# Kernel tuning notes

Hardware: AMD Instinct MI355X
Metric: run time of the kernel (lower is better)

Reference implementation:

```python
import jax, jax.numpy as jnp
import numpy as np

EMBED_DIM = 1024
NUM_HEADS = 16
HEAD_DIM = EMBED_DIM // NUM_HEADS
B, S = 4, 1024
EPS = 1e-5
NEG = -1e9


def layer_norm(h, gamma, beta):
    mu = jnp.mean(h, axis=-1, keepdims=True)
    var = jnp.mean(jnp.square(h - mu), axis=-1, keepdims=True)
    return (h - mu) * jax.lax.rsqrt(var + EPS) * gamma + beta


def setup_inputs() -> dict:
    key = jax.random.key(0)
    ks = jax.random.split(key, 8)
    scale = 1.0 / np.sqrt(EMBED_DIM)
    x = jax.random.normal(ks[0], (B, S, EMBED_DIM), dtype=jnp.float32)
    mask = jax.random.randint(ks[1], (B, S, S), 0, 2).astype(jnp.bool_)
    Wq = jax.random.uniform(ks[2], (EMBED_DIM, EMBED_DIM), jnp.float32, -scale, scale)
    bq = jax.random.uniform(ks[3], (EMBED_DIM,), jnp.float32, -scale, scale)
    Wk = jax.random.uniform(ks[4], (EMBED_DIM, EMBED_DIM), jnp.float32, -scale, scale)
    bk = jax.random.uniform(ks[5], (EMBED_DIM,), jnp.float32, -scale, scale)
    gq = jnp.ones((EMBED_DIM,), jnp.float32)
    bq_n = jnp.zeros((EMBED_DIM,), jnp.float32)
    gk = jnp.ones((EMBED_DIM,), jnp.float32)
    bk_n = jnp.zeros((EMBED_DIM,), jnp.float32)
    return {"x": x, "mask": mask, "Wq": Wq, "bq": bq, "Wk": Wk, "bk": bk,
            "gq": gq, "bq_n": bq_n, "gk": gk, "bk_n": bk_n}


def reference(x, mask, Wq, bq, Wk, bk, gq, bq_n, gk, bk_n):
    b, s, _ = x.shape
    # proj -> LayerNorm -> ReLU, split heads: [B,S,H,D]
    Q = jax.nn.relu(layer_norm(x @ Wq + bq, gq, bq_n)).reshape(b, s, NUM_HEADS, HEAD_DIM)
    K = jax.nn.relu(layer_norm(x @ Wk + bk, gk, bk_n)).reshape(b, s, NUM_HEADS, HEAD_DIM)
    # scores [B,H,S,S]
    scores = jnp.einsum('bqhd,bkhd->bhqk', Q, K) / np.sqrt(HEAD_DIM).astype(np.float32)
    # symmetric masking: mask applied along keys, then (via transpose trick) along queries
    m = (mask | jnp.swapaxes(mask, -1, -2))[:, None, :, :]
    scores = jnp.where(m, NEG, scores)
    attn = jax.nn.softmax(scores, axis=-1)
    return attn.mean(axis=1)  # [B,S,S]
```

## Files before the change

kernel.cpp:

```cpp
#include <hip/hip_runtime.h>
#include <hip/hip_bf16.h>

#define B_ 4
#define S_ 1024
#define E_ 1024
#define H_ 16
#define D_ 64

typedef __attribute__((ext_vector_type(8))) short short8;
typedef __attribute__((ext_vector_type(4))) float f32x4;

static __device__ __forceinline__ unsigned short f2bf(float x) {
  unsigned int u = __float_as_uint(x);
  unsigned int r = u + 0x7fffu + ((u >> 16) & 1u);
  return (unsigned short)(r >> 16);
}
static __device__ __forceinline__ float bf2f(unsigned short b) {
  return __uint_as_float((unsigned int)b << 16);
}

#define GL2LDS16(g, l)                                                            \
  __builtin_amdgcn_global_load_lds(                                               \
      (const __attribute__((address_space(1))) unsigned int*)(g),                 \
      (__attribute__((address_space(3))) unsigned int*)(l), 16, 0, 0)

__global__ __launch_bounds__(256) void prep_kernel(const int* __restrict__ mask,
                                                   const float* __restrict__ x,
                                                   const float* __restrict__ Wq,
                                                   const float* __restrict__ Wk,
                                                   unsigned char* __restrict__ msym,
                                                   unsigned short* __restrict__ xbf,
                                                   unsigned short* __restrict__ Wt) {
  __shared__ __align__(16) char u_lds[32 * 33 * 4];
  const int blk = blockIdx.x;
  const int tid = threadIdx.x;
  if (blk < 4096) {
    int (*T)[33] = (int(*)[33])u_lds;
    const int b = blk >> 10;
    const int rest = blk & 1023;
    const int i0 = (rest >> 5) << 5;
    const int j0 = (rest & 31) << 5;
    const int ii = tid >> 3;
    const int jj4 = (tid & 7) << 2;
    const size_t bO = (size_t)b * S_ * S_;
    const int4 m2 = *(const int4*)&mask[bO + (size_t)(j0 + ii) * S_ + i0 + jj4];
    T[ii][jj4 + 0] = m2.x; T[ii][jj4 + 1] = m2.y; T[ii][jj4 + 2] = m2.z; T[ii][jj4 + 3] = m2.w;
    __syncthreads();
    const int4 m1 = *(const int4*)&mask[bO + (size_t)(i0 + ii) * S_ + j0 + jj4];
    uchar4 o;
    o.x = ((m1.x != 0) || (T[jj4 + 0][ii] != 0)) ? 1 : 0;
    o.y = ((m1.y != 0) || (T[jj4 + 1][ii] != 0)) ? 1 : 0;
    o.z = ((m1.z != 0) || (T[jj4 + 2][ii] != 0)) ? 1 : 0;
    o.w = ((m1.w != 0) || (T[jj4 + 3][ii] != 0)) ? 1 : 0;
    *(uchar4*)&msym[bO + (size_t)(i0 + ii) * S_ + j0 + jj4] = o;
  } else if (blk < 6144) {
    const size_t i = ((size_t)(blk - 4096) * 256 + tid) * 8;
    const float4 a = *(const float4*)(x + i);
    const float4 b = *(const float4*)(x + i + 4);
    const ushort4 p0 = {f2bf(a.x), f2bf(a.y), f2bf(a.z), f2bf(a.w)};
    const ushort4 p1 = {f2bf(b.x), f2bf(b.y), f2bf(b.z), f2bf(b.w)};
    *(ushort4*)(xbf + i) = p0;
    *(ushort4*)(xbf + i + 4) = p1;
  } else {
    unsigned short (*T2)[36] = (unsigned short(*)[36])u_lds;
    const int wblk = blk - 6144;
    const int mat = wblk >> 10;
    const int kt = (wblk >> 5) & 31, ntb = wblk & 31;
    const float* W = mat ? Wk : Wq;
    const int r = tid >> 3, c4 = (tid & 7) << 2;
    const float4 v = *(const float4*)&W[(size_t)(kt * 32 + r) * 1024 + ntb * 32 + c4];
    T2[r][c4 + 0] = f2bf(v.x); T2[r][c4 + 1] = f2bf(v.y);
    T2[r][c4 + 2] = f2bf(v.z); T2[r][c4 + 3] = f2bf(v.w);
    __syncthreads();
    const ushort4 o = {T2[c4 + 0][r], T2[c4 + 1][r], T2[c4 + 2][r], T2[c4 + 3][r]};
    *(ushort4*)&Wt[(size_t)(mat * 1024 + ntb * 32 + r) * 1024 + kt * 32 + c4] = o;
  }
}

__global__ __launch_bounds__(256) void gemm_mfma_kernel(const unsigned short* __restrict__ Abf,
                                                        const unsigned short* __restrict__ Wt,
                                                        unsigned short* __restrict__ P,
                                                        int nstride) {
  __shared__ __align__(16) unsigned short As[128 * 32];
  __shared__ __align__(16) unsigned short Bs[128 * 32];
  const int tid = threadIdx.x;
  const int m0 = (blockIdx.x & 31) << 7;
  const int n0 = (blockIdx.x >> 5) << 7;
  const int wave = tid >> 6, lane = tid & 63;
  const int ln15 = lane & 15, rg = lane >> 4;
  const int wm = (wave & 1) << 6;
  const int wn = (wave >> 1) << 6;
  const int sr = tid >> 2;
  const int sc = (tid & 3) << 3;
  const unsigned short* gA = Abf + (size_t)(m0 + sr) * 1024 + sc;
  const unsigned short* gB = Wt + (size_t)(n0 + sr) * 1024 + sc;
  unsigned short* lA = As + tid * 8;
  unsigned short* lB = Bs + tid * 8;
  f32x4 acc[4][4];
#pragma unroll
  for (int i = 0; i < 4; ++i)
#pragma unroll
    for (int j = 0; j < 4; ++j) acc[i][j] = (f32x4){0.0f, 0.0f, 0.0f, 0.0f};

  const unsigned short* pa = As + (wm + ln15) * 32 + rg * 8;
  const unsigned short* pb = Bs + (wn + ln15) * 32 + rg * 8;
  for (int k0 = 0; k0 < E_; k0 += 32) {
    GL2LDS16(gA + k0, lA);
    GL2LDS16(gA + k0 + (size_t)64 * 1024, lA + 2048);
    GL2LDS16(gB + k0, lB);
    GL2LDS16(gB + k0 + (size_t)64 * 1024, lB + 2048);
    __syncthreads();
    short8 af[4], bfr[4];
#pragma unroll
    for (int i = 0; i < 4; ++i) af[i] = *(const short8*)(pa + i * 16 * 32);
#pragma unroll
    for (int j = 0; j < 4; ++j) bfr[j] = *(const short8*)(pb + j * 16 * 32);
#pragma unroll
    for (int i = 0; i < 4; ++i)
#pragma unroll
      for (int j = 0; j < 4; ++j)
        acc[i][j] = __builtin_amdgcn_mfma_f32_16x16x32_bf16(af[i], bfr[j], acc[i][j], 0, 0, 0);
    __syncthreads();
  }
#pragma unroll
  for (int i = 0; i < 4; ++i)
#pragma unroll
    for (int j = 0; j < 4; ++j)
#pragma unroll
      for (int r = 0; r < 4; ++r) {
        const int row = m0 + wm + i * 16 + rg * 4 + r;
        const int col = n0 + wn + j * 16 + ln15;
        P[(size_t)row * nstride + col] = f2bf(acc[i][j][r]);
      }
}

__global__ __launch_bounds__(256) void ln_relu_bf_kernel(const unsigned short* __restrict__ P,
                                                         int rowstride, int coloff,
                                                         const float* __restrict__ bias,
                                                         const float* __restrict__ gamma,
                                                         const float* __restrict__ beta,
                                                         unsigned short* __restrict__ obf) {
  const int row = blockIdx.x;
  const int b = row >> 10, s = row & 1023;
  const unsigned short* p = P + (size_t)row * rowstride + coloff;
  const int tid = threadIdx.x;
  const ushort4 pv = *(const ushort4*)(p + tid * 4);
  float4 v = {bf2f(pv.x), bf2f(pv.y), bf2f(pv.z), bf2f(pv.w)};
  const float4 bb = ((const float4*)bias)[tid];
  v.x += bb.x; v.y += bb.y; v.z += bb.z; v.w += bb.w;
  float sum = v.x + v.y + v.z + v.w;
  float s2 = v.x * v.x + v.y * v.y + v.z * v.z + v.w * v.w;
#pragma unroll
  for (int off = 32; off >= 1; off >>= 1) {
    sum += __shfl_xor(sum, off);
    s2 += __shfl_xor(s2, off);
  }
  __shared__ float red[2][4];
  const int wave = tid >> 6, lane = tid & 63;
  if (lane == 0) { red[0][wave] = sum; red[1][wave] = s2; }
  __syncthreads();
  sum = red[0][0] + red[0][1] + red[0][2] + red[0][3];
  s2 = red[1][0] + red[1][1] + red[1][2] + red[1][3];
  const float mu = sum * (1.0f / E_);
  const float var = s2 * (1.0f / E_) - mu * mu;
  const float r = rsqrtf(var + 1e-5f);
  const float4 g = ((const float4*)gamma)[tid];
  const float4 bt = ((const float4*)beta)[tid];
  const float o0 = fmaxf((v.x - mu) * r * g.x + bt.x, 0.0f);
  const float o1 = fmaxf((v.y - mu) * r * g.y + bt.y, 0.0f);
  const float o2 = fmaxf((v.z - mu) * r * g.z + bt.z, 0.0f);
  const float o3 = fmaxf((v.w - mu) * r * g.w + bt.w, 0.0f);
  const int h = tid >> 4;
  const int d = (tid & 15) << 2;
  const ushort4 ob = {f2bf(o0), f2bf(o1), f2bf(o2), f2bf(o3)};
  *(ushort4*)&obf[((size_t)(b * H_ + h) * S_ + s) * D_ + d] = ob;
}

__global__ __launch_bounds__(1024, 4) void attn5_kernel(const unsigned short* __restrict__ Qbf,
                                                        const unsigned short* __restrict__ Kbf,
                                                        const unsigned char* __restrict__ msym,
                                                        float* __restrict__ out) {
  __shared__ __align__(16) unsigned short Qs[256 * 64];
  __shared__ __align__(16) unsigned short Ks[2][256 * 64];
  __shared__ __align__(16) float l_lds[16][16];
  __shared__ __align__(16) float linv[16];
  const int tid = threadIdx.x;
  const int wave = tid >> 6, lane = tid & 63;
  const int ln15 = lane & 15, rg = lane >> 4;
  const int b = blockIdx.x & 3;
  const int q0 = (blockIdx.x >> 2) << 4;

  const unsigned short* Kb = Kbf + (size_t)b * H_ * S_ * D_;

  {
    const int rho = tid >> 3, p = tid & 7;
    const int c = p ^ (rho & 7);
    const int rho2 = rho + 128;
    const int c2 = p ^ (rho2 & 7);
    const uint4 v0 = *(const uint4*)(Qbf + ((size_t)(b * H_ + (rho >> 4)) * S_ + q0 + (rho & 15)) * D_ + c * 8);
    const uint4 v1 = *(const uint4*)(Qbf + ((size_t)(b * H_ + (rho2 >> 4)) * S_ + q0 + (rho2 & 15)) * D_ + c2 * 8);
    *(uint4*)&Qs[rho * 64 + p * 8] = v0;
    *(uint4*)&Qs[rho2 * 64 + p * 8] = v1;
  }
  unsigned int mbits = 0;
#pragma unroll
  for (int qt = 0; qt < 4; ++qt)
#pragma unroll
    for (int r = 0; r < 4; ++r)
      mbits |= (msym[((size_t)b * S_ + q0 + rg * 4 + r) * S_ + qt * 256 + wave * 16 + ln15] ? 1u : 0u)
               << (qt * 4 + r);

  const int krow = tid >> 3, kp = tid & 7;
  const int kcc = kp ^ (krow & 7);
  {
    const unsigned short* src = Kb + (size_t)krow * D_ + kcc * 8;
    const uint4 p0 = *(const uint4*)src;
    const uint4 p1 = *(const uint4*)(src + 128 * D_);
    *(uint4*)&Ks[0][krow * 64 + kp * 8] = p0;
    *(uint4*)&Ks[0][(krow + 128) * 64 + kp * 8] = p1;
  }
  __syncthreads();

  const int pfrag = (rg ^ (ln15 & 7)) * 8;
  const unsigned short* QsW = Qs + ln15 * 64;
  const unsigned short* KsW0 = Ks[0] + (wave * 16 + ln15) * 64;
  const unsigned short* KsW1 = Ks[1] + (wave * 16 + ln15) * 64;

  float o[4][4] = {};
  unsigned int epack[4][2];
  uint4 pf0, pf1;

#pragma unroll 1
  for (int h = 0; h < 16; ++h) {
    const unsigned short* qrow = QsW + h * 16 * 64;
    const short8 a0 = *(const short8*)(qrow + pfrag);
    const short8 a1 = *(const short8*)(qrow + (pfrag ^ 32));
    float la[4] = {0.0f, 0.0f, 0.0f, 0.0f};
#pragma unroll
    for (int qt = 0; qt < 4; ++qt) {
      const int s = h * 4 + qt;
      if (s < 63) {
        const int s1 = s + 1;
        const unsigned short* src =
            Kb + ((size_t)(s1 >> 2) * S_ + ((s1 & 3) << 8) + krow) * D_ + kcc * 8;
        pf0 = *(const uint4*)src;
        pf1 = *(const uint4*)(src + 128 * D_);
      }
      const unsigned short* kw = (qt & 1) ? KsW1 : KsW0;
      const short8 b0 = *(const short8*)(kw + pfrag);
      const short8 b1 = *(const short8*)(kw + (pfrag ^ 32));
      f32x4 cc = {0.0f, 0.0f, 0.0f, 0.0f};
      cc = __builtin_amdgcn_mfma_f32_16x16x32_bf16(a0, b0, cc, 0, 0, 0);
      cc = __builtin_amdgcn_mfma_f32_16x16x32_bf16(a1, b1, cc, 0, 0, 0);
      float e[4];
#pragma unroll
      for (int r = 0; r < 4; ++r) {
        const float sv = fminf(cc[r] * 0.125f, 80.0f);
        e[r] = ((mbits >> (qt * 4 + r)) & 1u) ? 0.0f : __expf(sv);
        la[r] += e[r];
      }
      epack[qt][0] = (unsigned)f2bf(e[0]) | ((unsigned)f2bf(e[1]) << 16);
      epack[qt][1] = (unsigned)f2bf(e[2]) | ((unsigned)f2bf(e[3]) << 16);
      if (s < 63) {
        unsigned short* dst = (qt & 1) ? Ks[0] : Ks[1];
        *(uint4*)&dst[krow * 64 + kp * 8] = pf0;
        *(uint4*)&dst[(krow + 128) * 64 + kp * 8] = pf1;
      }
      if (qt < 3) __syncthreads();
    }
#pragma unroll
    for (int r = 0; r < 4; ++r) {
      float lv = la[r];
      lv += __shfl_xor(lv, 1);
      lv += __shfl_xor(lv, 2);
      lv += __shfl_xor(lv, 4);
      lv += __shfl_xor(lv, 8);
      la[r] = lv;
    }
    if (ln15 == 0) *(float4*)&l_lds[wave][rg * 4] = (float4){la[0], la[1], la[2], la[3]};
    __syncthreads();
    if (tid < 16) {
      float ssum = 0.0f;
#pragma unroll
      for (int w = 0; w < 16; ++w) ssum += l_lds[w][tid];
      linv[tid] = 0.0625f / ssum;
    }
    __syncthreads();
    const float4 li4 = *(const float4*)&linv[rg * 4];
#pragma unroll
    for (int qt = 0; qt < 4; ++qt) {
      o[qt][0] += __uint_as_float(epack[qt][0] << 16) * li4.x;
      o[qt][1] += __uint_as_float(epack[qt][0] & 0xFFFF0000u) * li4.y;
      o[qt][2] += __uint_as_float(epack[qt][1] << 16) * li4.z;
      o[qt][3] += __uint_as_float(epack[qt][1] & 0xFFFF0000u) * li4.w;
    }
  }
#pragma unroll
  for (int qt = 0; qt < 4; ++qt)
#pragma unroll
    for (int r = 0; r < 4; ++r)
      out[((size_t)b * S_ + q0 + rg * 4 + r) * S_ + qt * 256 + wave * 16 + ln15] = o[qt][r];
}

extern "C" void kernel_launch(void* const* d_in, const int* in_sizes, int n_in,
                              void* d_out, int out_size, void* d_ws, size_t ws_size,
                              hipStream_t stream) {
  const float* x = (const float*)d_in[0];
  const int* mask = (const int*)d_in[1];
  const float* Wq = (const float*)d_in[2];
  const float* bq = (const float*)d_in[3];
  const float* Wk = (const float*)d_in[4];
  const float* bk = (const float*)d_in[5];
  const float* gq = (const float*)d_in[6];
  const float* bq_n = (const float*)d_in[7];
  const float* gk = (const float*)d_in[8];
  const float* bk_n = (const float*)d_in[9];
  float* out = (float*)d_out;

  char* ws = (char*)d_ws;
  const size_t MB = 1024 * 1024;

  if (ws_size >= 40 * MB) {
    unsigned short* P2 = (unsigned short*)ws;
    unsigned short* xbf = (unsigned short*)(ws + 16 * MB);
    unsigned short* Kbf = (unsigned short*)(ws + 16 * MB);
    unsigned short* Wt = (unsigned short*)(ws + 24 * MB);
    unsigned short* Qbf = (unsigned short*)(ws + 28 * MB);
    unsigned char* msym = (unsigned char*)(ws + 36 * MB);

    prep_kernel<<<8192, 256, 0, stream>>>(mask, x, Wq, Wk, msym, xbf, Wt);
    gemm_mfma_kernel<<<512, 256, 0, stream>>>(xbf, Wt, P2, 2048);
    ln_relu_bf_kernel<<<4096, 256, 0, stream>>>(P2, 2048, 0, bq, gq, bq_n, Qbf);
    ln_relu_bf_kernel<<<4096, 256, 0, stream>>>(P2, 2048, 1024, bk, gk, bk_n, Kbf);
    attn5_kernel<<<256, 1024, 0, stream>>>(Qbf, Kbf, msym, out);
  } else {
    unsigned short* P = (unsigned short*)ws;
    unsigned short* xbf = (unsigned short*)(ws + 8 * MB);
    unsigned short* Kbf = (unsigned short*)(ws + 8 * MB);
    unsigned short* Wt = (unsigned short*)(ws + 16 * MB);
    unsigned short* Qbf = (unsigned short*)(ws + 20 * MB);
    unsigned char* msym = (unsigned char*)(ws + 28 * MB);

    prep_kernel<<<8192, 256, 0, stream>>>(mask, x, Wq, Wk, msym, xbf, Wt);
    gemm_mfma_kernel<<<256, 256, 0, stream>>>(xbf, Wt, P, 1024);
    ln_relu_bf_kernel<<<4096, 256, 0, stream>>>(P, 1024, 0, bq, gq, bq_n, Qbf);
    gemm_mfma_kernel<<<256, 256, 0, stream>>>(xbf, Wt + (size_t)1024 * 1024, P, 1024);
    ln_relu_bf_kernel<<<4096, 256, 0, stream>>>(P, 1024, 0, bk, gk, bk_n, Kbf);
    attn5_kernel<<<256, 1024, 0, stream>>>(Qbf, Kbf, msym, out);
  }
}
```

Before: 201.6 us.

## Split attention heads across two blocks with atomic output accumulation; fuse Q/K layernorm launches

The attention kernel is split so each block handles 8 of the 16 heads with 512 threads instead of 16 heads with 1024. This doubles the grid to 512 blocks, and the two partial head-means are combined with atomicAdd into an output zeroed by a memset. The per-head softmax normalisation now uses a single barrier per tile, with row sums read directly from LDS, and the two layernorm launches are merged into one. The aim is better occupancy and parallelism, at the cost of an extra 16MB memset and atomic traffic on the 16MB output.

New measurement: 204.2 us. Within noise of the previous version (+1.3%).

```diff
diff --git a/kernel.cpp b/kernel.cpp
--- a/kernel.cpp
+++ b/kernel.cpp
@@ -134,16 +134,9 @@
       }
 }
 
-__global__ __launch_bounds__(256) void ln_relu_bf_kernel(const unsigned short* __restrict__ P,
-                                                         int rowstride, int coloff,
-                                                         const float* __restrict__ bias,
-                                                         const float* __restrict__ gamma,
-                                                         const float* __restrict__ beta,
-                                                         unsigned short* __restrict__ obf) {
-  const int row = blockIdx.x;
-  const int b = row >> 10, s = row & 1023;
-  const unsigned short* p = P + (size_t)row * rowstride + coloff;
-  const int tid = threadIdx.x;
+__device__ __forceinline__ void ln_body(const unsigned short* p, const float* bias,
+                                        const float* gamma, const float* beta,
+                                        unsigned short* obf, int b, int s, int tid) {
   const ushort4 pv = *(const ushort4*)(p + tid * 4);
   float4 v = {bf2f(pv.x), bf2f(pv.y), bf2f(pv.z), bf2f(pv.w)};
   const float4 bb = ((const float4*)bias)[tid];
@@ -176,77 +169,101 @@
   *(ushort4*)&obf[((size_t)(b * H_ + h) * S_ + s) * D_ + d] = ob;
 }
 
-__global__ __launch_bounds__(1024, 4) void attn5_kernel(const unsigned short* __restrict__ Qbf,
-                                                        const unsigned short* __restrict__ Kbf,
-                                                        const unsigned char* __restrict__ msym,
-                                                        float* __restrict__ out) {
-  __shared__ __align__(16) unsigned short Qs[256 * 64];
-  __shared__ __align__(16) unsigned short Ks[2][256 * 64];
-  __shared__ __align__(16) float l_lds[16][16];
-  __shared__ __align__(16) float linv[16];
+__global__ __launch_bounds__(256) void ln_relu_bf_kernel(const unsigned short* __restrict__ P,
+                                                         int rowstride, int coloff,
+                                                         const float* __restrict__ bias,
+                                                         const float* __restrict__ gamma,
+                                                         const float* __restrict__ beta,
+                                                         unsigned short* __restrict__ obf) {
+  const int row = blockIdx.x;
+  ln_body(P + (size_t)row * rowstride + coloff, bias, gamma, beta, obf,
+          row >> 10, row & 1023, threadIdx.x);
+}
+
+__global__ __launch_bounds__(256) void ln2_kernel(const unsigned short* __restrict__ P2,
+                                                  const float* __restrict__ bq,
+                                                  const float* __restrict__ gq,
+                                                  const float* __restrict__ bqn,
+                                                  const float* __restrict__ bk,
+                                                  const float* __restrict__ gk,
+                                                  const float* __restrict__ bkn,
+                                                  unsigned short* __restrict__ Qbf,
+                                                  unsigned short* __restrict__ Kbf) {
+  const int blk = blockIdx.x;
+  const int sel = blk >> 12;
+  const int row = blk & 4095;
+  ln_body(P2 + (size_t)row * 2048 + sel * 1024,
+          sel ? bk : bq, sel ? gk : gq, sel ? bkn : bqn,
+          sel ? Kbf : Qbf, row >> 10, row & 1023, threadIdx.x);
+}
+
+__global__ __launch_bounds__(512, 4) void attn6_kernel(const unsigned short* __restrict__ Qbf,
+                                                       const unsigned short* __restrict__ Kbf,
+                                                       const unsigned char* __restrict__ msym,
+                                                       float* __restrict__ out) {
+  __shared__ __align__(16) unsigned short Qs[128 * 64];
+  __shared__ __align__(16) unsigned short Ks[2][128 * 64];
+  __shared__ __align__(16) float l_lds[16][8];
   const int tid = threadIdx.x;
   const int wave = tid >> 6, lane = tid & 63;
   const int ln15 = lane & 15, rg = lane >> 4;
   const int b = blockIdx.x & 3;
-  const int q0 = (blockIdx.x >> 2) << 4;
-
-  const unsigned short* Kb = Kbf + (size_t)b * H_ * S_ * D_;
+  const int hh = (blockIdx.x >> 2) & 1;
+  const int q0 = (blockIdx.x >> 3) << 4;
+  const unsigned short* Kb = Kbf + (size_t)(b * H_ + hh * 8) * S_ * D_;
 
   {
-    const int rho = tid >> 3, p = tid & 7;
-    const int c = p ^ (rho & 7);
-    const int rho2 = rho + 128;
-    const int c2 = p ^ (rho2 & 7);
-    const uint4 v0 = *(const uint4*)(Qbf + ((size_t)(b * H_ + (rho >> 4)) * S_ + q0 + (rho & 15)) * D_ + c * 8);
-    const uint4 v1 = *(const uint4*)(Qbf + ((size_t)(b * H_ + (rho2 >> 4)) * S_ + q0 + (rho2 & 15)) * D_ + c2 * 8);
-    *(uint4*)&Qs[rho * 64 + p * 8] = v0;
-    *(uint4*)&Qs[rho2 * 64 + p * 8] = v1;
+    const int rho = tid >> 2;
+    const int c0 = (tid & 3) << 1;
+    const int x = rho & 7;
+    const unsigned short* src =
+        Qbf + ((size_t)(b * H_ + hh * 8 + (rho >> 4)) * S_ + q0 + (rho & 15)) * D_ + c0 * 8;
+    const uint4 v0 = *(const uint4*)src;
+    const uint4 v1 = *(const uint4*)(src + 8);
+    *(uint4*)&Qs[rho * 64 + (c0 ^ x) * 8] = v0;
+    *(uint4*)&Qs[rho * 64 + ((c0 + 1) ^ x) * 8] = v1;
+  }
+  const int krow = tid >> 2, kc0 = (tid & 3) << 1;
+  const int kx = krow & 7;
+  const int kp0 = (kc0 ^ kx) * 8, kp1 = ((kc0 + 1) ^ kx) * 8;
+  {
+    const unsigned short* src = Kb + (size_t)krow * D_ + kc0 * 8;
+    const uint4 p0 = *(const uint4*)src;
+    const uint4 p1 = *(const uint4*)(src + 8);
+    *(uint4*)&Ks[0][krow * 64 + kp0] = p0;
+    *(uint4*)&Ks[0][krow * 64 + kp1] = p1;
   }
   unsigned int mbits = 0;
 #pragma unroll
-  for (int qt = 0; qt < 4; ++qt)
+  for (int t = 0; t < 8; ++t)
 #pragma unroll
     for (int r = 0; r < 4; ++r)
-      mbits |= (msym[((size_t)b * S_ + q0 + rg * 4 + r) * S_ + qt * 256 + wave * 16 + ln15] ? 1u : 0u)
-               << (qt * 4 + r);
-
-  const int krow = tid >> 3, kp = tid & 7;
-  const int kcc = kp ^ (krow & 7);
-  {
-    const unsigned short* src = Kb + (size_t)krow * D_ + kcc * 8;
-    const uint4 p0 = *(const uint4*)src;
-    const uint4 p1 = *(const uint4*)(src + 128 * D_);
-    *(uint4*)&Ks[0][krow * 64 + kp * 8] = p0;
-    *(uint4*)&Ks[0][(krow + 128) * 64 + kp * 8] = p1;
-  }
+      mbits |= (msym[((size_t)b * S_ + q0 + rg * 4 + r) * S_ + t * 128 + wave * 16 + ln15] ? 1u : 0u)
+               << (t * 4 + r);
   __syncthreads();
 
   const int pfrag = (rg ^ (ln15 & 7)) * 8;
-  const unsigned short* QsW = Qs + ln15 * 64;
-  const unsigned short* KsW0 = Ks[0] + (wave * 16 + ln15) * 64;
-  const unsigned short* KsW1 = Ks[1] + (wave * 16 + ln15) * 64;
-
-  float o[4][4] = {};
-  unsigned int epack[4][2];
-  uint4 pf0, pf1;
+  float o[8][4] = {};
 
 #pragma unroll 1
-  for (int h = 0; h < 16; ++h) {
-    const unsigned short* qrow = QsW + h * 16 * 64;
+  for (int hl = 0; hl < 8; ++hl) {
+    const unsigned short* qrow = Qs + (hl * 16 + ln15) * 64;
     const short8 a0 = *(const short8*)(qrow + pfrag);
     const short8 a1 = *(const short8*)(qrow + (pfrag ^ 32));
     float la[4] = {0.0f, 0.0f, 0.0f, 0.0f};
-#pragma unroll
-    for (int qt = 0; qt < 4; ++qt) {
-      const int s = h * 4 + qt;
-      if (s < 63) {
-        const int s1 = s + 1;
+    unsigned int epack[8][2];
+#pragma unroll
+    for (int t = 0; t < 8; ++t) {
+      const bool more = (t < 7) || (hl < 7);
+      uint4 pf0, pf1;
+      if (more) {
+        const int s1 = hl * 8 + t + 1;
         const unsigned short* src =
-            Kb + ((size_t)(s1 >> 2) * S_ + ((s1 & 3) << 8) + krow) * D_ + kcc * 8;
+            Kb + ((size_t)(s1 >> 3) * S_ + ((s1 & 7) << 7) + krow) * D_ + kc0 * 8;
         pf0 = *(const uint4*)src;
-        pf1 = *(const uint4*)(src + 128 * D_);
-      }
-      const unsigned short* kw = (qt & 1) ? KsW1 : KsW0;
+        pf1 = *(const uint4*)(src + 8);
+      }
+      const unsigned short* kw = Ks[t & 1] + (wave * 16 + ln15) * 64;
       const short8 b0 = *(const short8*)(kw + pfrag);
       const short8 b1 = *(const short8*)(kw + (pfrag ^ 32));
       f32x4 cc = {0.0f, 0.0f, 0.0f, 0.0f};
@@ -256,50 +273,53 @@
 #pragma unroll
       for (int r = 0; r < 4; ++r) {
         const float sv = fminf(cc[r] * 0.125f, 80.0f);
-        e[r] = ((mbits >> (qt * 4 + r)) & 1u) ? 0.0f : __expf(sv);
+        e[r] = ((mbits >> (t * 4 + r)) & 1u) ? 0.0f : __expf(sv);
         la[r] += e[r];
       }
-      epack[qt][0] = (unsigned)f2bf(e[0]) | ((unsigned)f2bf(e[1]) << 16);
-      epack[qt][1] = (unsigned)f2bf(e[2]) | ((unsigned)f2bf(e[3]) << 16);
-      if (s < 63) {
-        unsigned short* dst = (qt & 1) ? Ks[0] : Ks[1];
-        *(uint4*)&dst[krow * 64 + kp * 8] = pf0;
-        *(uint4*)&dst[(krow + 128) * 64 + kp * 8] = pf1;
-      }
-      if (qt < 3) __syncthreads();
+      epack[t][0] = (unsigned)f2bf(e[0]) | ((unsigned)f2bf(e[1]) << 16);
+      epack[t][1] = (unsigned)f2bf(e[2]) | ((unsigned)f2bf(e[3]) << 16);
+      if (t == 7) {
+#pragma unroll
+        for (int r = 0; r < 4; ++r) {
+          float lv = la[r];
+          lv += __shfl_xor(lv, 1);
+          lv += __shfl_xor(lv, 2);
+          lv += __shfl_xor(lv, 4);
+          lv += __shfl_xor(lv, 8);
+          la[r] = lv;
+        }
+        if (ln15 == 0) {
+#pragma unroll
+          for (int r = 0; r < 4; ++r) l_lds[rg * 4 + r][wave] = la[r];
+        }
+      }
+      if (more) {
+        unsigned short* dst = Ks[(t + 1) & 1];
+        *(uint4*)&dst[krow * 64 + kp0] = pf0;
+        *(uint4*)&dst[krow * 64 + kp1] = pf1;
+      }
+      __syncthreads();
     }
 #pragma unroll
     for (int r = 0; r < 4; ++r) {
-      float lv = la[r];
-      lv += __shfl_xor(lv, 1);
-      lv += __shfl_xor(lv, 2);
-      lv += __shfl_xor(lv, 4);
-      lv += __shfl_xor(lv, 8);
-      la[r] = lv;
+      const float4 va = *(const float4*)&l_lds[rg * 4 + r][0];
+      const float4 vb = *(const float4*)&l_lds[rg * 4 + r][4];
+      const float ssum = ((va.x + va.y) + (va.z + va.w)) + ((vb.x + vb.y) + (vb.z + vb.w));
+      const float li = 0.0625f * __builtin_amdgcn_rcpf(ssum);
+#pragma unroll
+      for (int t = 0; t < 8; ++t) {
+        const unsigned u = epack[t][r >> 1];
+        const float ev = (r & 1) ? __uint_as_float(u & 0xFFFF0000u) : __uint_as_float(u << 16);
+        o[t][r] += ev * li;
+      }
     }
-    if (ln15 == 0) *(float4*)&l_lds[wave][rg * 4] = (float4){la[0], la[1], la[2], la[3]};
-    __syncthreads();
-    if (tid < 16) {
-      float ssum = 0.0f;
-#pragma unroll
-      for (int w = 0; w < 16; ++w) ssum += l_lds[w][tid];
-      linv[tid] = 0.0625f / ssum;
-    }
-    __syncthreads();
-    const float4 li4 = *(const float4*)&linv[rg * 4];
-#pragma unroll
-    for (int qt = 0; qt < 4; ++qt) {
-      o[qt][0] += __uint_as_float(epack[qt][0] << 16) * li4.x;
-      o[qt][1] += __uint_as_float(epack[qt][0] & 0xFFFF0000u) * li4.y;
-      o[qt][2] += __uint_as_float(epack[qt][1] << 16) * li4.z;
-      o[qt][3] += __uint_as_float(epack[qt][1] & 0xFFFF0000u) * li4.w;
-    }
-  }
-#pragma unroll
-  for (int qt = 0; qt < 4; ++qt)
+  }
+#pragma unroll
+  for (int t = 0; t < 8; ++t)
 #pragma unroll
     for (int r = 0; r < 4; ++r)
-      out[((size_t)b * S_ + q0 + rg * 4 + r) * S_ + qt * 256 + wave * 16 + ln15] = o[qt][r];
+      atomicAdd(&out[((size_t)b * S_ + q0 + rg * 4 + r) * S_ + t * 128 + wave * 16 + ln15],
+                o[t][r]);
 }
 
 extern "C" void kernel_launch(void* const* d_in, const int* in_sizes, int n_in,
@@ -330,9 +350,9 @@
 
     prep_kernel<<<8192, 256, 0, stream>>>(mask, x, Wq, Wk, msym, xbf, Wt);
     gemm_mfma_kernel<<<512, 256, 0, stream>>>(xbf, Wt, P2, 2048);
-    ln_relu_bf_kernel<<<4096, 256, 0, stream>>>(P2, 2048, 0, bq, gq, bq_n, Qbf);
-    ln_relu_bf_kernel<<<4096, 256, 0, stream>>>(P2, 2048, 1024, bk, gk, bk_n, Kbf);
-    attn5_kernel<<<256, 1024, 0, stream>>>(Qbf, Kbf, msym, out);
+    ln2_kernel<<<8192, 256, 0, stream>>>(P2, bq, gq, bq_n, bk, gk, bk_n, Qbf, Kbf);
+    hipMemsetAsync(out, 0, (size_t)B_ * S_ * S_ * sizeof(float), stream);
+    attn6_kernel<<<512, 512, 0, stream>>>(Qbf, Kbf, msym, out);
   } else {
     unsigned short* P = (unsigned short*)ws;
     unsigned short* xbf = (unsigned short*)(ws + 8 * MB);
@@ -346,6 +366,7 @@
     ln_relu_bf_kernel<<<4096, 256, 0, stream>>>(P, 1024, 0, bq, gq, bq_n, Qbf);
     gemm_mfma_kernel<<<256, 256, 0, stream>>>(xbf, Wt + (size_t)1024 * 1024, P, 1024);
     ln_relu_bf_kernel<<<4096, 256, 0, stream>>>(P, 1024, 0, bk, gk, bk_n, Kbf);
-    attn5_kernel<<<256, 1024, 0, stream>>>(Qbf, Kbf, msym, out);
-  }
-}
+    hipMemsetAsync(out, 0, (size_t)B_ * S_ * S_ * sizeof(float), stream);
+    attn6_kernel<<<512, 512, 0, stream>>>(Qbf, Kbf, msym, out);
+  }
+}
```
